# Kernel tuning notes

Hardware: AMD Instinct MI355X
Metric: run time of the kernel (lower is better)

The kernel has to match this reference:

```python
import jax, jax.numpy as jnp
import numpy as np


def setup_inputs() -> dict:
    key = jax.random.key(0)
    ks = jax.random.split(key, 14)
    B, S, C, R = 4, 2048, 1024, 4
    s = 0.02
    inp = {
        "hidden_states": jax.random.normal(ks[0], (B, S, C), jnp.float32),
        "Wq": jax.random.normal(ks[1], (C, C), jnp.float32) * s,
        "Wk": jax.random.normal(ks[2], (C, C), jnp.float32) * s,
        "Wv": jax.random.normal(ks[3], (C, C), jnp.float32) * s,
        "Wo": jax.random.normal(ks[4], (C, C), jnp.float32) * s,
        "bo": jnp.zeros((C,), jnp.float32),
        "q_down": jax.random.normal(ks[5], (R, C), jnp.float32) * (1.0 / R),
        "q_up": jnp.zeros((C, R), jnp.float32) + jax.random.normal(ks[6], (C, R), jnp.float32) * s,
        "k_down": jax.random.normal(ks[7], (R, C), jnp.float32) * (1.0 / R),
        "k_up": jax.random.normal(ks[8], (C, R), jnp.float32) * s,
        "v_down": jax.random.normal(ks[9], (R, C), jnp.float32) * (1.0 / R),
        "v_up": jax.random.normal(ks[10], (C, R), jnp.float32) * s,
        "o_down": jax.random.normal(ks[11], (R, C), jnp.float32) * (1.0 / R),
        "o_up": jax.random.normal(ks[12], (C, R), jnp.float32) * s,
        "num_heads": 16,
    }
    return inp


def _lora_linear(x, W, down, up, scale):
    # base Linear (no bias) + lora_scale * up(down(x))
    base = jnp.einsum("bsc,oc->bso", x, W)
    low = jnp.einsum("bsc,rc->bsr", x, down)
    return base + scale * jnp.einsum("bsr,or->bso", low, up)


def reference(hidden_states, Wq, Wk, Wv, Wo, bo,
              q_down, q_up, k_down, k_up, v_down, v_up, o_down, o_up,
              num_heads):
    B, S, C = hidden_states.shape
    H = num_heads
    D = C // H
    lora_scale = 1.0

    q = _lora_linear(hidden_states, Wq, q_down, q_up, lora_scale)
    k = _lora_linear(hidden_states, Wk, k_down, k_up, lora_scale)
    v = _lora_linear(hidden_states, Wv, v_down, v_up, lora_scale)

    # head_to_batch_dim: [B,S,C] -> [B,H,S,D]
    q = q.reshape(B, S, H, D).transpose(0, 2, 1, 3)
    k = k.reshape(B, S, H, D).transpose(0, 2, 1, 3)
    v = v.reshape(B, S, H, D).transpose(0, 2, 1, 3)

    scale = 1.0 / jnp.sqrt(jnp.asarray(D, hidden_states.dtype))
    scores = jnp.einsum("bhsd,bhtd->bhst", q, k) * scale  # [B,H,S,S]
    probs = jax.nn.softmax(scores, axis=-1)
    out = jnp.einsum("bhst,bhtd->bhsd", probs, v)

    # batch_to_head_dim: [B,H,S,D] -> [B,S,C]
    out = out.transpose(0, 2, 1, 3).reshape(B, S, C)

    out = _lora_linear(out, Wo, o_down, o_up, lora_scale) + bo
    return out
```

## Files before the change

### kernel.cpp

```cpp
#include <hip/hip_runtime.h>
#include <stdint.h>

typedef __attribute__((ext_vector_type(8))) short short8;
typedef __attribute__((ext_vector_type(4))) float f32x4;

typedef const unsigned int __attribute__((address_space(1))) gu32;
typedef unsigned int __attribute__((address_space(3))) lu32;

__device__ __forceinline__ float bf2f(unsigned short u) {
  union { unsigned int i; float f; } v; v.i = ((unsigned int)u) << 16; return v.f;
}
__device__ __forceinline__ unsigned short f2bf(float f) {
  union { float f; unsigned int i; } v; v.f = f;
  unsigned int r = v.i + 0x7FFFu + ((v.i >> 16) & 1u);
  return (unsigned short)(r >> 16);
}
__device__ __forceinline__ float fexp2(float x) {
  float r; asm("v_exp_f32 %0, %1" : "=v"(r) : "v"(x)); return r;
}
__device__ __forceinline__ unsigned int cvtpk(float lo, float hi) {
  unsigned int r;
  asm("v_cvt_pk_bf16_f32 %0, %1, %2" : "=v"(r) : "v"(lo), "v"(hi));
  return r;
}

__global__ __launch_bounds__(256) void fold_w(
    const float* __restrict__ Wq, const float* __restrict__ Wk,
    const float* __restrict__ Wv, const float* __restrict__ Wo,
    const float* __restrict__ qd, const float* __restrict__ qu,
    const float* __restrict__ kd, const float* __restrict__ ku,
    const float* __restrict__ vd, const float* __restrict__ vu,
    const float* __restrict__ od, const float* __restrict__ ou,
    unsigned short* __restrict__ Wqkv, unsigned short* __restrict__ Wob)
{
  int idx = blockIdx.x * 256 + threadIdx.x;
  int sel = idx >> 20;
  int rem = idx & 0xFFFFF;
  int o = rem >> 10, c = rem & 1023;
  const float *W, *up, *dn;
  if (sel == 0)      { W = Wq; up = qu; dn = qd; }
  else if (sel == 1) { W = Wk; up = ku; dn = kd; }
  else if (sel == 2) { W = Wv; up = vu; dn = vd; }
  else               { W = Wo; up = ou; dn = od; }
  float acc = W[rem];
  #pragma unroll
  for (int r = 0; r < 4; r++) acc += up[o * 4 + r] * dn[r * 1024 + c];
  if (sel < 3) Wqkv[sel * 1048576 + rem] = f2bf(acc);
  else         Wob[rem] = f2bf(acc);
}

__global__ __launch_bounds__(256) void cvt_x(const float* __restrict__ X,
                                             unsigned short* __restrict__ Xb)
{
  int i = (blockIdx.x * 256 + threadIdx.x) * 4;
  float4 v = *(const float4*)&X[i];
  unsigned short o0 = f2bf(v.x), o1 = f2bf(v.y), o2 = f2bf(v.z), o3 = f2bf(v.w);
  unsigned long long pk = (unsigned long long)o0 | ((unsigned long long)o1 << 16) |
                          ((unsigned long long)o2 << 32) | ((unsigned long long)o3 << 48);
  *(unsigned long long*)&Xb[i] = pk;
}

template <int OUTF>
__global__ __launch_bounds__(256) void gemm_bt(
    const unsigned short* __restrict__ A, const unsigned short* __restrict__ B,
    unsigned short* __restrict__ Cb, float* __restrict__ Cf,
    const float* __restrict__ bias, int M, int N, int K)
{
  __shared__ unsigned short smA[128 * 32];
  __shared__ unsigned short smB[128 * 32];
  const int tid = threadIdx.x;
  const int w = tid >> 6, lane = tid & 63;
  const int g = lane >> 4, lr = lane & 15;
  const int m0 = blockIdx.y * 128, n0 = blockIdx.x * 128;
  const int srow = lane >> 2;
  const int scol = (lane & 3) * 8;
  const unsigned short* gA = A + (size_t)(m0 + w * 16 + srow) * K + scol;
  const unsigned short* gB = B + (size_t)(n0 + w * 16 + srow) * K + scol;
  f32x4 acc[4][4] = {};
  const int wr = (w >> 1) * 64, wc = (w & 1) * 64;

  for (int k0 = 0; k0 < K; k0 += 32) {
    #pragma unroll
    for (int i = 0; i < 2; i++) {
      __builtin_amdgcn_global_load_lds((gu32*)(gA + (size_t)i * 64 * K + k0),
          (lu32*)&smA[(i * 64 + w * 16) * 32], 16, 0, 0);
      __builtin_amdgcn_global_load_lds((gu32*)(gB + (size_t)i * 64 * K + k0),
          (lu32*)&smB[(i * 64 + w * 16) * 32], 16, 0, 0);
    }
    __syncthreads();
    short8 a[4], b[4];
    #pragma unroll
    for (int mi = 0; mi < 4; mi++) a[mi] = *(const short8*)&smA[(wr + mi * 16 + lr) * 32 + g * 8];
    #pragma unroll
    for (int ni = 0; ni < 4; ni++) b[ni] = *(const short8*)&smB[(wc + ni * 16 + lr) * 32 + g * 8];
    #pragma unroll
    for (int mi = 0; mi < 4; mi++)
      #pragma unroll
      for (int ni = 0; ni < 4; ni++)
        acc[mi][ni] = __builtin_amdgcn_mfma_f32_16x16x32_bf16(a[mi], b[ni], acc[mi][ni], 0, 0, 0);
    __syncthreads();
  }

  #pragma unroll
  for (int mi = 0; mi < 4; mi++) {
    #pragma unroll
    for (int ni = 0; ni < 4; ni++) {
      int col = n0 + wc + ni * 16 + lr;
      #pragma unroll
      for (int j = 0; j < 4; j++) {
        int row = m0 + wr + mi * 16 + g * 4 + j;
        if (OUTF == 0) Cb[(size_t)row * N + col] = f2bf(acc[mi][ni][j]);
        else           Cf[(size_t)row * N + col] = acc[mi][ni][j] + bias[col];
      }
    }
  }
}

__global__ __launch_bounds__(256) void prep_kv(
    const unsigned short* __restrict__ QKV,
    unsigned short* __restrict__ Kswz, unsigned short* __restrict__ VTs)
{
  __shared__ unsigned short vt[64 * 72];
  int bh = blockIdx.x;
  int st = blockIdx.y;
  int b = bh >> 4, h = bh & 15;
  int s0 = st * 64;
  int tid = threadIdx.x;
  #pragma unroll
  for (int i = 0; i < 2; i++) {
    int idx = tid + i * 256;
    int r = idx >> 3, gch = idx & 7;
    size_t rowg = (size_t)(b * 2048 + s0 + r) * 3072;
    short8 kv = *(const short8*)&QKV[rowg + 1024 + h * 64 + gch * 8];
    int gout = gch ^ (r & 7);
    *(short8*)&Kswz[(size_t)(bh * 2048 + s0 + r) * 64 + gout * 8] = kv;
    short8 vv = *(const short8*)&QKV[rowg + 2048 + h * 64 + gch * 8];
    *(short8*)&vt[r * 72 + gch * 8] = vv;
  }
  __syncthreads();
  #pragma unroll
  for (int i = 0; i < 2; i++) {
    int idx = tid + i * 256;
    int d = idx >> 3, gp = idx & 7;
    int gs = gp ^ (d & 7);
    short8 o;
    #pragma unroll
    for (int j = 0; j < 8; j++) o[j] = (short)vt[(gs * 8 + j) * 72 + d];
    *(short8*)&VTs[(size_t)(bh * 64 + d) * 2048 + s0 + gp * 8] = o;
  }
}

__global__ __launch_bounds__(512, 4) void attn(
    const unsigned short* __restrict__ QKV,
    const unsigned short* __restrict__ Kswz,
    const unsigned short* __restrict__ VTs,
    unsigned short* __restrict__ O)
{
  __shared__ unsigned short smK[2][64 * 64];
  __shared__ unsigned short smV[2][64 * 64];
  __shared__ unsigned short smP[8][32 * 64];
  int qb = blockIdx.x, bh = blockIdx.y;
  int b = bh >> 4, h = bh & 15;
  int tid = threadIdx.x, w = tid >> 6, lane = tid & 63;
  int g = lane >> 4, lr = lane & 15;
  int q0 = qb * 256 + w * 32;
  const size_t kbse = (size_t)bh * 2048 * 64;
  const size_t vbse = (size_t)bh * 64 * 2048;
  const int srow8 = lane >> 3;
  const int sc8 = (lane & 7) * 8;

  auto stage = [&](int buf, int n0) {
    const unsigned short* gk = &Kswz[kbse + (size_t)(n0 + w * 8 + srow8) * 64 + sc8];
    __builtin_amdgcn_global_load_lds((gu32*)gk, (lu32*)&smK[buf][(w * 8) * 64], 16, 0, 0);
    const unsigned short* gv = &VTs[vbse + (size_t)(w * 8 + srow8) * 2048 + n0 + sc8];
    __builtin_amdgcn_global_load_lds((gu32*)gv, (lu32*)&smV[buf][(w * 8) * 64], 16, 0, 0);
  };

  stage(0, 0);

  const float SC = 0.125f * 1.44269504f;
  short8 bq[2][2];
  #pragma unroll
  for (int qf = 0; qf < 2; qf++)
    #pragma unroll
    for (int ks = 0; ks < 2; ks++) {
      short8 v = *(const short8*)&QKV[(size_t)(b * 2048 + q0 + qf * 16 + lr) * 3072 +
                                      h * 64 + ks * 32 + g * 8];
      #pragma unroll
      for (int j = 0; j < 4; j++) {
        float f0 = bf2f((unsigned short)v[2 * j]) * SC;
        float f1 = bf2f((unsigned short)v[2 * j + 1]) * SC;
        ((unsigned int*)&v)[j] = cvtpk(f0, f1);
      }
      bq[qf][ks] = v;
    }

  short8 vones;
  #pragma unroll
  for (int j = 0; j < 8; j++) vones[j] = (short)0x3F80;

  f32x4 acc_o[2][4] = {};
  f32x4 acc_l[2] = {};

  __syncthreads();

  for (int t = 0; t < 32; t++) {
    int cur = t & 1;
    if (t < 31) stage(cur ^ 1, (t + 1) * 64);

    f32x4 s[4][2] = {};
    __builtin_amdgcn_s_setprio(1);
    #pragma unroll
    for (int nf = 0; nf < 4; nf++) {
      int row = nf * 16 + lr;
      #pragma unroll
      for (int ks = 0; ks < 2; ks++) {
        int eo = (ks * 64 + g * 16) ^ ((row & 7) << 4);
        short8 ak = *(const short8*)&smK[cur][row * 64 + (eo >> 1)];
        #pragma unroll
        for (int qf = 0; qf < 2; qf++)
          s[nf][qf] = __builtin_amdgcn_mfma_f32_16x16x32_bf16(ak, bq[qf][ks], s[nf][qf], 0, 0, 0);
      }
    }
    __builtin_amdgcn_s_setprio(0);

    #pragma unroll
    for (int qf = 0; qf < 2; qf++) {
      int q = qf * 16 + lr;
      #pragma unroll
      for (int nf = 0; nf < 4; nf++) {
        float p0 = fexp2(s[nf][qf][0]);
        float p1 = fexp2(s[nf][qf][1]);
        float p2 = fexp2(s[nf][qf][2]);
        float p3 = fexp2(s[nf][qf][3]);
        uint2 pw;
        pw.x = cvtpk(p0, p1);
        pw.y = cvtpk(p2, p3);
        int eo = ((nf * 16 + g * 4) * 2) ^ ((q & 7) << 4);
        *(uint2*)&smP[w][q * 64 + (eo >> 1)] = pw;
      }
    }

    __builtin_amdgcn_s_setprio(1);
    #pragma unroll
    for (int ks = 0; ks < 2; ks++) {
      short8 ap[2];
      #pragma unroll
      for (int mq = 0; mq < 2; mq++) {
        int q = mq * 16 + lr;
        int eo = (ks * 64 + g * 16) ^ ((q & 7) << 4);
        ap[mq] = *(const short8*)&smP[w][q * 64 + (eo >> 1)];
        acc_l[mq] = __builtin_amdgcn_mfma_f32_16x16x32_bf16(ap[mq], vones, acc_l[mq], 0, 0, 0);
      }
      #pragma unroll
      for (int df = 0; df < 4; df++) {
        int d = df * 16 + lr;
        int eo = (ks * 64 + g * 16) ^ ((d & 7) << 4);
        short8 bv = *(const short8*)&smV[cur][d * 64 + (eo >> 1)];
        #pragma unroll
        for (int mq = 0; mq < 2; mq++)
          acc_o[mq][df] = __builtin_amdgcn_mfma_f32_16x16x32_bf16(ap[mq], bv, acc_o[mq][df], 0, 0, 0);
      }
    }
    __builtin_amdgcn_s_setprio(0);

    __syncthreads();
  }

  #pragma unroll
  for (int mq = 0; mq < 2; mq++)
    #pragma unroll
    for (int j = 0; j < 4; j++) {
      float inv = 1.0f / acc_l[mq][j];
      #pragma unroll
      for (int df = 0; df < 4; df++) {
        int row = b * 2048 + q0 + mq * 16 + g * 4 + j;
        int col = h * 64 + df * 16 + lr;
        O[(size_t)row * 1024 + col] = f2bf(acc_o[mq][df][j] * inv);
      }
    }
}

extern "C" void kernel_launch(void* const* d_in, const int* in_sizes, int n_in,
                              void* d_out, int out_size, void* d_ws, size_t ws_size,
                              hipStream_t stream) {
  const float* X  = (const float*)d_in[0];
  const float* Wq = (const float*)d_in[1];
  const float* Wk = (const float*)d_in[2];
  const float* Wv = (const float*)d_in[3];
  const float* Wo = (const float*)d_in[4];
  const float* bo = (const float*)d_in[5];
  const float* qd = (const float*)d_in[6];
  const float* qu = (const float*)d_in[7];
  const float* kd = (const float*)d_in[8];
  const float* ku = (const float*)d_in[9];
  const float* vd = (const float*)d_in[10];
  const float* vu = (const float*)d_in[11];
  const float* od = (const float*)d_in[12];
  const float* ou = (const float*)d_in[13];

  char* ws = (char*)d_ws;
  unsigned short* Wqkv = (unsigned short*)(ws);
  unsigned short* Wob  = (unsigned short*)(ws + 6291456);
  unsigned short* Xb   = (unsigned short*)(ws + 8388608);
  unsigned short* QKV  = (unsigned short*)(ws + 25165824);
  unsigned short* Kswz = (unsigned short*)(ws + 75497472);
  unsigned short* VTs  = (unsigned short*)(ws + 92274688);

  fold_w<<<16384, 256, 0, stream>>>(Wq, Wk, Wv, Wo, qd, qu, kd, ku, vd, vu, od, ou, Wqkv, Wob);
  cvt_x<<<8192, 256, 0, stream>>>(X, Xb);
  gemm_bt<0><<<dim3(24, 64), 256, 0, stream>>>(Xb, Wqkv, QKV, nullptr, nullptr, 8192, 3072, 1024);
  prep_kv<<<dim3(64, 32), 256, 0, stream>>>(QKV, Kswz, VTs);
  attn<<<dim3(8, 64), 512, 0, stream>>>(QKV, Kswz, VTs, Xb);
  gemm_bt<1><<<dim3(8, 64), 256, 0, stream>>>(Xb, Wob, nullptr, (float*)d_out, bo, 8192, 1024, 1024);
}
```

Baseline: 208.6 us.

## Triple-buffer LDS staging with one barrier per step in GEMM and attention

Both the projection GEMM and the attention kernel now keep three LDS buffers and issue global-to-LDS loads two tiles ahead. Each step synchronises with a counted vmcnt wait plus a single s_barrier, replacing the two __syncthreads per iteration. The goal is to hide global load latency behind MFMA work and cut barrier stalls. In exchange it uses more LDS per block, which may lower occupancy, especially for attention with 512-thread blocks and launch_bounds(512,4). It also depends on hand-written waitcnt values matching the number of outstanding loads.

```diff
diff --git a/kernel.cpp b/kernel.cpp
--- a/kernel.cpp
+++ b/kernel.cpp
@@ -66,8 +66,8 @@
     unsigned short* __restrict__ Cb, float* __restrict__ Cf,
     const float* __restrict__ bias, int M, int N, int K)
 {
-  __shared__ unsigned short smA[128 * 32];
-  __shared__ unsigned short smB[128 * 32];
+  __shared__ unsigned short smA[3][128 * 32];
+  __shared__ unsigned short smB[3][128 * 32];
   const int tid = threadIdx.x;
   const int w = tid >> 6, lane = tid & 63;
   const int g = lane >> 4, lr = lane & 15;
@@ -79,27 +79,57 @@
   f32x4 acc[4][4] = {};
   const int wr = (w >> 1) * 64, wc = (w & 1) * 64;
 
-  for (int k0 = 0; k0 < K; k0 += 32) {
+  auto stage = [&](int buf, int k0) {
     #pragma unroll
     for (int i = 0; i < 2; i++) {
       __builtin_amdgcn_global_load_lds((gu32*)(gA + (size_t)i * 64 * K + k0),
-          (lu32*)&smA[(i * 64 + w * 16) * 32], 16, 0, 0);
+          (lu32*)&smA[buf][(i * 64 + w * 16) * 32], 16, 0, 0);
       __builtin_amdgcn_global_load_lds((gu32*)(gB + (size_t)i * 64 * K + k0),
-          (lu32*)&smB[(i * 64 + w * 16) * 32], 16, 0, 0);
-    }
-    __syncthreads();
+          (lu32*)&smB[buf][(i * 64 + w * 16) * 32], 16, 0, 0);
+    }
+  };
+  auto compute = [&](int buf) {
     short8 a[4], b[4];
     #pragma unroll
-    for (int mi = 0; mi < 4; mi++) a[mi] = *(const short8*)&smA[(wr + mi * 16 + lr) * 32 + g * 8];
-    #pragma unroll
-    for (int ni = 0; ni < 4; ni++) b[ni] = *(const short8*)&smB[(wc + ni * 16 + lr) * 32 + g * 8];
+    for (int mi = 0; mi < 4; mi++) a[mi] = *(const short8*)&smA[buf][(wr + mi * 16 + lr) * 32 + g * 8];
+    #pragma unroll
+    for (int ni = 0; ni < 4; ni++) b[ni] = *(const short8*)&smB[buf][(wc + ni * 16 + lr) * 32 + g * 8];
     #pragma unroll
     for (int mi = 0; mi < 4; mi++)
       #pragma unroll
       for (int ni = 0; ni < 4; ni++)
         acc[mi][ni] = __builtin_amdgcn_mfma_f32_16x16x32_bf16(a[mi], b[ni], acc[mi][ni], 0, 0, 0);
-    __syncthreads();
-  }
+  };
+
+  const int nt = K / 32;
+  stage(0, 0);
+  stage(1, 32);
+  int cur = 0;
+  for (int t = 0; t + 2 < nt; ++t) {
+    asm volatile("s_waitcnt vmcnt(4)" ::: "memory");
+    __builtin_amdgcn_sched_barrier(0);
+    __builtin_amdgcn_s_barrier();
+    __builtin_amdgcn_sched_barrier(0);
+    int nb = (cur == 0) ? 2 : cur - 1;
+    stage(nb, (t + 2) * 32);
+    compute(cur);
+    asm volatile("s_waitcnt lgkmcnt(0)" ::: "memory");
+    __builtin_amdgcn_sched_barrier(0);
+    cur = (cur == 2) ? 0 : cur + 1;
+  }
+  asm volatile("s_waitcnt vmcnt(4)" ::: "memory");
+  __builtin_amdgcn_sched_barrier(0);
+  __builtin_amdgcn_s_barrier();
+  __builtin_amdgcn_sched_barrier(0);
+  compute(cur);
+  asm volatile("s_waitcnt lgkmcnt(0)" ::: "memory");
+  __builtin_amdgcn_sched_barrier(0);
+  cur = (cur == 2) ? 0 : cur + 1;
+  asm volatile("s_waitcnt vmcnt(0)" ::: "memory");
+  __builtin_amdgcn_sched_barrier(0);
+  __builtin_amdgcn_s_barrier();
+  __builtin_amdgcn_sched_barrier(0);
+  compute(cur);
 
   #pragma unroll
   for (int mi = 0; mi < 4; mi++) {
@@ -156,8 +186,8 @@
     const unsigned short* __restrict__ VTs,
     unsigned short* __restrict__ O)
 {
-  __shared__ unsigned short smK[2][64 * 64];
-  __shared__ unsigned short smV[2][64 * 64];
+  __shared__ unsigned short smK[3][64 * 64];
+  __shared__ unsigned short smV[3][64 * 64];
   __shared__ unsigned short smP[8][32 * 64];
   int qb = blockIdx.x, bh = blockIdx.y;
   int b = bh >> 4, h = bh & 15;
@@ -176,8 +206,6 @@
     __builtin_amdgcn_global_load_lds((gu32*)gv, (lu32*)&smV[buf][(w * 8) * 64], 16, 0, 0);
   };
 
-  stage(0, 0);
-
   const float SC = 0.125f * 1.44269504f;
   short8 bq[2][2];
   #pragma unroll
@@ -202,12 +230,14 @@
   f32x4 acc_o[2][4] = {};
   f32x4 acc_l[2] = {};
 
-  __syncthreads();
-
-  for (int t = 0; t < 32; t++) {
-    int cur = t & 1;
-    if (t < 31) stage(cur ^ 1, (t + 1) * 64);
-
+  asm volatile("s_waitcnt vmcnt(0)" ::: "memory");
+  __builtin_amdgcn_sched_barrier(0);
+  stage(0, 0);
+  stage(1, 64);
+
+  auto compute = [&](int buf) {
+    const unsigned short* K_ = smK[buf];
+    const unsigned short* V_ = smV[buf];
     f32x4 s[4][2] = {};
     __builtin_amdgcn_s_setprio(1);
     #pragma unroll
@@ -216,7 +246,7 @@
       #pragma unroll
       for (int ks = 0; ks < 2; ks++) {
         int eo = (ks * 64 + g * 16) ^ ((row & 7) << 4);
-        short8 ak = *(const short8*)&smK[cur][row * 64 + (eo >> 1)];
+        short8 ak = *(const short8*)&K_[row * 64 + (eo >> 1)];
         #pragma unroll
         for (int qf = 0; qf < 2; qf++)
           s[nf][qf] = __builtin_amdgcn_mfma_f32_16x16x32_bf16(ak, bq[qf][ks], s[nf][qf], 0, 0, 0);
@@ -256,16 +286,41 @@
       for (int df = 0; df < 4; df++) {
         int d = df * 16 + lr;
         int eo = (ks * 64 + g * 16) ^ ((d & 7) << 4);
-        short8 bv = *(const short8*)&smV[cur][d * 64 + (eo >> 1)];
+        short8 bv = *(const short8*)&V_[d * 64 + (eo >> 1)];
         #pragma unroll
         for (int mq = 0; mq < 2; mq++)
           acc_o[mq][df] = __builtin_amdgcn_mfma_f32_16x16x32_bf16(ap[mq], bv, acc_o[mq][df], 0, 0, 0);
       }
     }
     __builtin_amdgcn_s_setprio(0);
-
-    __syncthreads();
-  }
+  };
+
+  int cur = 0;
+  for (int t = 0; t + 2 < 32; ++t) {
+    asm volatile("s_waitcnt vmcnt(2)" ::: "memory");
+    __builtin_amdgcn_sched_barrier(0);
+    __builtin_amdgcn_s_barrier();
+    __builtin_amdgcn_sched_barrier(0);
+    int nb = (cur == 0) ? 2 : cur - 1;
+    stage(nb, (t + 2) * 64);
+    compute(cur);
+    asm volatile("s_waitcnt lgkmcnt(0)" ::: "memory");
+    __builtin_amdgcn_sched_barrier(0);
+    cur = (cur == 2) ? 0 : cur + 1;
+  }
+  asm volatile("s_waitcnt vmcnt(2)" ::: "memory");
+  __builtin_amdgcn_sched_barrier(0);
+  __builtin_amdgcn_s_barrier();
+  __builtin_amdgcn_sched_barrier(0);
+  compute(cur);
+  asm volatile("s_waitcnt lgkmcnt(0)" ::: "memory");
+  __builtin_amdgcn_sched_barrier(0);
+  cur = (cur == 2) ? 0 : cur + 1;
+  asm volatile("s_waitcnt vmcnt(0)" ::: "memory");
+  __builtin_amdgcn_sched_barrier(0);
+  __builtin_amdgcn_s_barrier();
+  __builtin_amdgcn_sched_barrier(0);
+  compute(cur);
 
   #pragma unroll
   for (int mq = 0; mq < 2; mq++)
```

Result: faster. 200.7 us (-3.8%).
